# Kernel tuning notes

Hardware: AMD Instinct MI355X
Metric: run time of the kernel (lower is better)

## Reference

```python
import jax, jax.numpy as jnp
import numpy as np

DG = 8   # deformable groups
KK = 9   # 3x3 kernel positions


def conv3x3(x, w, b):
    # x: [B,C,H,W], w: [O,I,3,3] -> SAME conv, stride 1
    y = jax.lax.conv_general_dilated(x, w, (1, 1), 'SAME',
                                     dimension_numbers=('NCHW', 'OIHW', 'NCHW'))
    return y + b[None, :, None, None]


def modulated_deform_conv(x, offset, mask, w, b):
    # x: [B,C,H,W]; offset: [B,DG,KK,2,H,W] (dy,dx per group/kernel-pos);
    # mask: [B,DG,KK,H,W]; w: [O,C,3,3]; groups=1, stride=1, pad=1, dil=1.
    B, C, H, W = x.shape
    cg = C // DG  # channels per deformable group
    dy = offset[:, :, :, 0]  # [B,DG,KK,H,W]
    dx = offset[:, :, :, 1]
    ky, kx = jnp.meshgrid(jnp.arange(3), jnp.arange(3), indexing='ij')
    ky = (ky.reshape(KK) - 1).astype(x.dtype)  # kernel y offsets (pad=1)
    kx = (kx.reshape(KK) - 1).astype(x.dtype)
    py = dy + jnp.arange(H, dtype=x.dtype).reshape(1, 1, 1, H, 1) + ky.reshape(1, 1, KK, 1, 1)
    px = dx + jnp.arange(W, dtype=x.dtype).reshape(1, 1, 1, 1, W) + kx.reshape(1, 1, KK, 1, 1)
    y0 = jnp.floor(py)
    x0 = jnp.floor(px)
    ly = py - y0  # bilinear fractions
    lx = px - x0
    y0i = y0.astype(jnp.int32)
    x0i = x0.astype(jnp.int32)
    xf = x.reshape(B, DG, cg, H * W)

    def gather(yi, xi):
        # zero padding outside the image (per-corner validity)
        valid = ((yi >= 0) & (yi < H) & (xi >= 0) & (xi < W)).astype(x.dtype)
        idx = jnp.clip(yi, 0, H - 1) * W + jnp.clip(xi, 0, W - 1)  # [B,DG,KK,H,W]
        g = jnp.take_along_axis(xf, idx.reshape(B, DG, 1, KK * H * W), axis=-1)
        return g.reshape(B, DG, cg, KK, H, W) * valid[:, :, None]

    v = (((1 - ly) * (1 - lx))[:, :, None] * gather(y0i, x0i)
         + ((1 - ly) * lx)[:, :, None] * gather(y0i, x0i + 1)
         + (ly * (1 - lx))[:, :, None] * gather(y0i + 1, x0i)
         + (ly * lx)[:, :, None] * gather(y0i + 1, x0i + 1))
    v = (v * mask[:, :, None]).reshape(B, C, KK, H, W)  # modulated im2col
    out = jnp.einsum('bckhw,ock->bohw', v, w.reshape(w.shape[0], C, KK))
    return out + b[None, :, None, None]


def setup_inputs() -> dict:
    key = jax.random.key(0)
    ks = jax.random.split(key, 6)
    B, C, H, W = 8, 64, 128, 128
    f = lambda k, s: jax.random.normal(k, s, dtype=jnp.float32)
    return {
        'cat_fea': f(ks[0], (B, C, H, W)),
        'f_fea': f(ks[1], (B, C, H, W)),
        'w_off2d': f(ks[2], (C, C, 3, 3)) * 0.05,
        'b_off2d': jnp.zeros((C,), jnp.float32),
        'w_coff': f(ks[3], (3 * DG * KK, C, 3, 3)) * 0.01,  # small => near-zero offsets, as in DCNv2Pack init
        'b_coff': jnp.zeros((3 * DG * KK,), jnp.float32),
        'w_dconv': f(ks[4], (C, C, 3, 3)) * 0.05,
        'b_dconv': jnp.zeros((C,), jnp.float32),
    }


def reference(cat_fea, f_fea, w_off2d, b_off2d, w_coff, b_coff, w_dconv, b_dconv):
    # offset1 = self.off2d_1(cat_fea)
    offset_feat = conv3x3(cat_fea, w_off2d, b_off2d)
    # DCNv2Pack: conv_offset on the extra feature, chunk into o1,o2,mask
    off = conv3x3(offset_feat, w_coff, b_coff)  # [B, 3*DG*KK, H, W]
    o1, o2, m = jnp.split(off, 3, axis=1)
    B, _, H, W = off.shape
    # offset = cat(o1,o2); CUDA kernel reads channel ((g*KK+i)*2 + {0:y,1:x})
    offset = jnp.concatenate([o1, o2], axis=1).reshape(B, DG, KK, 2, H, W)
    mask = jax.nn.sigmoid(m).reshape(B, DG, KK, H, W)
    return modulated_deform_conv(f_fea, offset, mask, w_dconv, b_dconv)
```

## Files before the change

kernel.cpp:

```cpp
#include <hip/hip_runtime.h>
#include <math.h>

typedef __attribute__((ext_vector_type(4))) float f32x4;
typedef __attribute__((ext_vector_type(8))) short bf16x8;
typedef __attribute__((ext_vector_type(2))) _Float16 f16x2;
typedef __attribute__((ext_vector_type(8))) _Float16 f16x8;

#define HH 128
#define WW 128
#define HWSZ 16384
#define BHW 131072
#define BB 8

__device__ __forceinline__ float bf2f(ushort u) {
    union { uint i; float f; } x; x.i = ((uint)u) << 16; return x.f;
}
__device__ __forceinline__ ushort f2bf(float f) {
    union { float f; uint i; } x; x.f = f;
    uint r = (x.i + 0x7fffu + ((x.i >> 16) & 1u)) >> 16;
    return (ushort)r;
}
__device__ __forceinline__ ushort f2h_bits(float f) {
    union { _Float16 h; ushort u; } x; x.h = (_Float16)f; return x.u;
}

template<int F16>
__global__ __launch_bounds__(256) void to_gp_k(const float* __restrict__ x,
                                               ushort* __restrict__ y) {
    __shared__ ushort lds[64][66];
    int blk = blockIdx.x;
    int b = blk >> 8;
    int hw0 = (blk & 255) << 6;
    int t = threadIdx.x;
    int lane = t & 63;
    int q = t >> 6;
#pragma unroll
    for (int i = 0; i < 16; i++) {
        int c = i * 4 + q;
        float v = x[((size_t)(b * 64 + c) << 14) + hw0 + lane];
        lds[c][lane] = F16 ? f2h_bits(v) : f2bf(v);
    }
    __syncthreads();
#pragma unroll
    for (int it = 0; it < 2; it++) {
        int id = it * 256 + t;
        int cg = id >> 6;
        int px = id & 63;
        uint pk[4];
#pragma unroll
        for (int j = 0; j < 4; j++)
            pk[j] = (uint)lds[cg * 8 + 2 * j][px] | ((uint)lds[cg * 8 + 2 * j + 1][px] << 16);
        *(uint4*)(y + ((((size_t)b * 8 + cg) << 14) + hw0 + px) * 8) = *(uint4*)pk;
    }
}

template<int F16>
__global__ __launch_bounds__(256) void prep_wa(const float* __restrict__ w,
                                               ushort* __restrict__ wa, int Co, int Co_pad) {
    int idx = blockIdx.x * 256 + threadIdx.x;
    if (idx >= Co_pad * 576) return;
    int co = idx / 576, r = idx % 576;
    int kk = r >> 6, ci = r & 63;
    ushort v = 0;
    if (co < Co) {
        float f = w[(co * 64 + ci) * 9 + kk];
        v = F16 ? f2h_bits(f) : f2bf(f);
    }
    wa[idx] = v;
}

template<int NCO, int MODE>
__global__ __launch_bounds__(256, 3) void conv_gemm2_k(
    const ushort* __restrict__ xt, const ushort* __restrict__ wa,
    const float* __restrict__ bias, ushort* __restrict__ y,
    uint* __restrict__ dyxp, ushort* __restrict__ mpl, int Cout) {
    __shared__ ushort Al[NCO * 64 * 64];
    __shared__ ushort Bt[64 * 64];
    int t = threadIdx.x;
    int orig = blockIdx.x;
    int blk = (orig & 7) * 256 + (orig >> 3);
    int b = blk >> 8;
    int h = (blk >> 1) & 127;
    int w0 = (blk & 1) << 6;
    int lane = t & 63;
    int wv = t >> 6;
    int lg = lane >> 4;
    int lr = lane & 15;
    int rs = (lr & 7) << 4;
    int asw = ((lane & 7) ^ (lane >> 3)) << 4;
    const char* wab = (const char*)wa;

    f32x4 acc[NCO][4];
#pragma unroll
    for (int n = 0; n < NCO; n++)
#pragma unroll
        for (int j = 0; j < 4; j++) acc[n][j] = f32x4{0, 0, 0, 0};

#pragma unroll 1
    for (int kk = 0; kk < 9; kk++) {
        int ky = kk / 3;
        int kx = kk - ky * 3;
        __syncthreads();
#pragma unroll
        for (int a = 0; a < 2 * NCO; a++) {
            int rb = wv * (NCO * 16) + a * 8;
            const char* g = wab + (size_t)(rb + (lane >> 3)) * 1152 + kk * 128 + asw;
            __builtin_amdgcn_global_load_lds(
                (const __attribute__((address_space(1))) void*)g,
                (__attribute__((address_space(3))) void*)((char*)Al + rb * 128),
                16, 0, 0);
        }
        int hy = h + ky - 1;
        int wx = w0 + lane + kx - 1;
        bool val = ((unsigned)hy < 128u) && ((unsigned)wx < 128u);
        uint4 v0 = {0u, 0u, 0u, 0u}, v1 = {0u, 0u, 0u, 0u};
        if (val) {
            const ushort* gb = xt + ((((size_t)b * 8 + wv) << 14) + (hy << 7) + wx) * 8;
            v0 = *(const uint4*)gb;
            v1 = *(const uint4*)(gb + (4ull << 17));
        }
        int swl = (lane & 7) << 4;
        *(uint4*)((char*)Bt + lane * 128 + ((wv * 16) ^ swl)) = v0;
        *(uint4*)((char*)Bt + lane * 128 + (((wv + 4) * 16) ^ swl)) = v1;
        __syncthreads();
#pragma unroll
        for (int n = 0; n < NCO; n++) {
            int ar = n * 64 + wv * 16 + lr;
            bf16x8 a0 = *(const bf16x8*)((char*)Al + ar * 128 + ((lg * 16) ^ rs));
            bf16x8 a1 = *(const bf16x8*)((char*)Al + ar * 128 + ((lg * 16 + 64) ^ rs));
#pragma unroll
            for (int j = 0; j < 4; j++) {
                int pr = j * 16 + lr;
                bf16x8 b0 = *(const bf16x8*)((char*)Bt + pr * 128 + ((lg * 16) ^ rs));
                bf16x8 b1 = *(const bf16x8*)((char*)Bt + pr * 128 + ((lg * 16 + 64) ^ rs));
                acc[n][j] = __builtin_amdgcn_mfma_f32_16x16x32_bf16(a0, b0, acc[n][j], 0, 0, 0);
                acc[n][j] = __builtin_amdgcn_mfma_f32_16x16x32_bf16(a1, b1, acc[n][j], 0, 0, 0);
            }
        }
    }

#pragma unroll
    for (int n = 0; n < NCO; n++) {
        int co_g = n * 64 + wv * 16 + lg * 4;
        if (co_g < Cout) {
            float bs[4];
#pragma unroll
            for (int r = 0; r < 4; r++) bs[r] = bias[co_g + r];
#pragma unroll
            for (int j = 0; j < 4; j++) {
                int pxl = j * 16 + lr;
                int hw = (h << 7) + w0 + pxl;
                int bhw = (b << 14) + hw;
                if (MODE == 0) {
                    int cg = co_g >> 3, cs = co_g & 7;
                    uint2 s2;
                    s2.x = (uint)f2bf(acc[n][j][0] + bs[0]) | ((uint)f2bf(acc[n][j][1] + bs[1]) << 16);
                    s2.y = (uint)f2bf(acc[n][j][2] + bs[2]) | ((uint)f2bf(acc[n][j][3] + bs[3]) << 16);
                    *(uint2*)(y + ((((size_t)b * 8 + cg) << 14) + hw) * 8 + cs) = s2;
                } else if (co_g < 144) {
                    int p0 = co_g >> 1;
                    uint u0 = (uint)f2bf(acc[n][j][0] + bs[0]) | ((uint)f2bf(acc[n][j][1] + bs[1]) << 16);
                    uint u1 = (uint)f2bf(acc[n][j][2] + bs[2]) | ((uint)f2bf(acc[n][j][3] + bs[3]) << 16);
                    dyxp[(size_t)p0 * BHW + bhw] = u0;
                    dyxp[(size_t)(p0 + 1) * BHW + bhw] = u1;
                } else {
#pragma unroll
                    for (int r = 0; r < 4; r++) {
                        float f = 1.f / (1.f + __expf(-(acc[n][j][r] + bs[r])));
                        mpl[(size_t)(co_g - 144 + r) * BHW + bhw] = f2bf(f);
                    }
                }
            }
        }
    }
}

__global__ __launch_bounds__(256) void sample_k(
    const ushort* __restrict__ xg, const uint* __restrict__ dyxp,
    const ushort* __restrict__ mpl, ushort* __restrict__ vt) {
    int p = blockIdx.y;
    int dg = p / 9, tap = p - dg * 9;
    int ky = tap / 3, kx = tap - ky * 3;
    int bx = blockIdx.x;
    int bxs = (bx & 7) * 64 + (bx >> 3);
    int bhw = (bxs << 8) + threadIdx.x;
    int b = bhw >> 14;
    int h = (bhw >> 7) & 127;
    int w = bhw & 127;

    uint dyx = dyxp[(size_t)p * BHW + bhw];
    float m = bf2f(mpl[(size_t)p * BHW + bhw]);
    float dy = bf2f((ushort)(dyx & 0xffff));
    float dx = bf2f((ushort)(dyx >> 16));
    float py = dy + (float)(h + ky - 1);
    float px_ = dx + (float)(w + kx - 1);
    float fy = floorf(py), fx = floorf(px_);
    int y0 = (int)fy, x0 = (int)fx;
    int y1 = y0 + 1, x1 = x0 + 1;
    float ly = py - fy, lx = px_ - fx;
    bool vy0 = (unsigned)y0 < 128u, vy1 = (unsigned)y1 < 128u;
    bool vx0 = (unsigned)x0 < 128u, vx1 = (unsigned)x1 < 128u;
    float w00 = (vy0 && vx0) ? (1.f - ly) * (1.f - lx) * m : 0.f;
    float w01 = (vy0 && vx1) ? (1.f - ly) * lx * m : 0.f;
    float w10 = (vy1 && vx0) ? ly * (1.f - lx) * m : 0.f;
    float w11 = (vy1 && vx1) ? ly * lx * m : 0.f;
    int y0c = min(max(y0, 0), 127), y1c = min(max(y1, 0), 127);
    int x0c = min(max(x0, 0), 127), x1c = min(max(x1, 0), 127);
    const ushort* gb = xg + (((size_t)b * 8 + dg) << 17);
    uint4 q00 = *(const uint4*)(gb + ((y0c << 7) + x0c) * 8);
    uint4 q01 = *(const uint4*)(gb + ((y0c << 7) + x1c) * 8);
    uint4 q10 = *(const uint4*)(gb + ((y1c << 7) + x0c) * 8);
    uint4 q11 = *(const uint4*)(gb + ((y1c << 7) + x1c) * 8);
    const ushort* u00 = (const ushort*)&q00;
    const ushort* u01 = (const ushort*)&q01;
    const ushort* u10 = (const ushort*)&q10;
    const ushort* u11 = (const ushort*)&q11;
    uint pk[4];
#pragma unroll
    for (int c2 = 0; c2 < 4; c2++) {
        float v0 = w00 * bf2f(u00[2*c2])   + w01 * bf2f(u01[2*c2])
                 + w10 * bf2f(u10[2*c2])   + w11 * bf2f(u11[2*c2]);
        float v1 = w00 * bf2f(u00[2*c2+1]) + w01 * bf2f(u01[2*c2+1])
                 + w10 * bf2f(u10[2*c2+1]) + w11 * bf2f(u11[2*c2+1]);
        pk[c2] = (uint)f2bf(v0) | ((uint)f2bf(v1) << 16);
    }
    *(uint4*)(vt + ((size_t)p * BHW + bhw) * 8) = *(uint4*)pk;
}

__global__ __launch_bounds__(256, 3) void dgemm_k(
    const ushort* __restrict__ vt, const ushort* __restrict__ wa,
    const float* __restrict__ bias, float* __restrict__ out) {
    __shared__ ushort Al[64 * 64];
    __shared__ ushort Bt[64 * 64];
    int t = threadIdx.x;
    int orig = blockIdx.x;
    int blk = (orig & 7) * 256 + (orig >> 3);
    int b = blk >> 8;
    int h = (blk >> 1) & 127;
    int w0 = (blk & 1) << 6;
    int lane = t & 63;
    int wv = t >> 6;
    int lg = lane >> 4;
    int lr = lane & 15;
    int rs = (lr & 7) << 4;
    int asw = ((lane & 7) ^ (lane >> 3)) << 4;
    const char* wab = (const char*)wa;
    int bhw0 = (b << 14) + (h << 7) + w0;

    f32x4 acc[4] = {f32x4{0,0,0,0}, f32x4{0,0,0,0}, f32x4{0,0,0,0}, f32x4{0,0,0,0}};

#pragma unroll 1
    for (int kk = 0; kk < 9; kk++) {
        __syncthreads();
#pragma unroll
        for (int a = 0; a < 2; a++) {
            int rb = wv * 16 + a * 8;
            const char* g = wab + (size_t)(rb + (lane >> 3)) * 1152 + kk * 128 + asw;
            __builtin_amdgcn_global_load_lds(
                (const __attribute__((address_space(1))) void*)g,
                (__attribute__((address_space(3))) void*)((char*)Al + rb * 128),
                16, 0, 0);
        }
        uint4 v0 = *(const uint4*)(vt + ((size_t)(wv * 9 + kk) * BHW + bhw0 + lane) * 8);
        uint4 v1 = *(const uint4*)(vt + ((size_t)((wv + 4) * 9 + kk) * BHW + bhw0 + lane) * 8);
        int swl = (lane & 7) << 4;
        *(uint4*)((char*)Bt + lane * 128 + ((wv * 16) ^ swl)) = v0;
        *(uint4*)((char*)Bt + lane * 128 + (((wv + 4) * 16) ^ swl)) = v1;
        __syncthreads();
        int ar = wv * 16 + lr;
        bf16x8 a0 = *(const bf16x8*)((char*)Al + ar * 128 + ((lg * 16) ^ rs));
        bf16x8 a1 = *(const bf16x8*)((char*)Al + ar * 128 + ((lg * 16 + 64) ^ rs));
#pragma unroll
        for (int j = 0; j < 4; j++) {
            int pr = j * 16 + lr;
            bf16x8 b0 = *(const bf16x8*)((char*)Bt + pr * 128 + ((lg * 16) ^ rs));
            bf16x8 b1 = *(const bf16x8*)((char*)Bt + pr * 128 + ((lg * 16 + 64) ^ rs));
            acc[j] = __builtin_amdgcn_mfma_f32_16x16x32_bf16(a0, b0, acc[j], 0, 0, 0);
            acc[j] = __builtin_amdgcn_mfma_f32_16x16x32_bf16(a1, b1, acc[j], 0, 0, 0);
        }
    }

    int co_g = wv * 16 + lg * 4;
    float bs[4];
#pragma unroll
    for (int r = 0; r < 4; r++) bs[r] = bias[co_g + r];
#pragma unroll
    for (int j = 0; j < 4; j++) {
        int hw = (h << 7) + w0 + j * 16 + lr;
#pragma unroll
        for (int r = 0; r < 4; r++) {
            out[((size_t)(b * 64 + co_g + r) << 14) + hw] = acc[j][r] + bs[r];
        }
    }
}

__global__ __launch_bounds__(256, 3) void deform_reg3_k(
    const ushort* __restrict__ xg, const uint* __restrict__ dyxp,
    const ushort* __restrict__ mpl, const ushort* __restrict__ wa,
    const float* __restrict__ bias, float* __restrict__ out) {
    int t = threadIdx.x;
    int orig = blockIdx.x;
    int blk = (orig & 7) * 256 + (orig >> 3);
    int b = blk >> 8;
    int h = (blk >> 1) & 127;
    int w0 = (blk & 1) << 6;
    int lane = t & 63;
    int wv = t >> 6;
    int lg = lane >> 4;
    int lr = lane & 15;
    int wabs = w0 + wv * 16 + lr;
    int bhw = (b << 14) + (h << 7) + wabs;

    uint dyxv[18];
    float mv[18];
#pragma unroll
    for (int c = 0; c < 18; c++) {
        int dg = ((c & 1) << 2) + lg;
        int tap = c >> 1;
        dyxv[c] = dyxp[(size_t)(dg * 9 + tap) * BHW + bhw];
        mv[c] = bf2f(mpl[(size_t)(dg * 9 + tap) * BHW + bhw]);
    }

    uint4 qg[2][4];
    f32x4 wt4[2];
    f16x8 afr[2][4];
    f32x4 acc[4] = {f32x4{0,0,0,0}, f32x4{0,0,0,0}, f32x4{0,0,0,0}, f32x4{0,0,0,0}};

#define DPRE(c) do {                                                            \
    const int tap = (c) >> 1;                                                   \
    const int ky = tap / 3;                                                     \
    const int kx = tap - ky * 3;                                                \
    int dg = (((c) & 1) << 2) + lg;                                             \
    uint dyx = dyxv[(c)];                                                       \
    float dy = bf2f((ushort)(dyx & 0xffff));                                    \
    float dx = bf2f((ushort)(dyx >> 16));                                       \
    float py = dy + (float)(h + ky - 1);                                        \
    float px_ = dx + (float)(wabs + kx - 1);                                    \
    float fy = floorf(py), fx = floorf(px_);                                    \
    int y0 = (int)fy, x0 = (int)fx;                                             \
    int y1 = y0 + 1, x1 = x0 + 1;                                               \
    int y0c = min(max(y0, 0), 127), y1c = min(max(y1, 0), 127);                 \
    int x0c = min(max(x0, 0), 127), x1c = min(max(x1, 0), 127);                 \
    const ushort* gb = xg + (((size_t)b * 8 + dg) << 17);                       \
    qg[(c) & 1][0] = *(const uint4*)(gb + ((y0c << 7) + x0c) * 8);              \
    qg[(c) & 1][1] = *(const uint4*)(gb + ((y0c << 7) + x1c) * 8);              \
    qg[(c) & 1][2] = *(const uint4*)(gb + ((y1c << 7) + x0c) * 8);              \
    qg[(c) & 1][3] = *(const uint4*)(gb + ((y1c << 7) + x1c) * 8);              \
    float ly = py - fy, lx = px_ - fx;                                          \
    bool vy0 = (unsigned)y0 < 128u, vy1 = (unsigned)y1 < 128u;                  \
    bool vx0 = (unsigned)x0 < 128u, vx1 = (unsigned)x1 < 128u;                  \
    float m = mv[(c)];                                                          \
    f32x4 wv4;                                                                  \
    wv4[0] = (vy0 && vx0) ? (1.f - ly) * (1.f - lx) * m : 0.f;                  \
    wv4[1] = (vy0 && vx1) ? (1.f - ly) * lx * m : 0.f;                          \
    wv4[2] = (vy1 && vx0) ? ly * (1.f - lx) * m : 0.f;                          \
    wv4[3] = (vy1 && vx1) ? ly * lx * m : 0.f;                                  \
    wt4[(c) & 1] = wv4;                                                         \
} while (0)

#define APRE(c) do {                                                            \
    const ushort* wac = wa + (c) * 32 + lg * 8;                                 \
    _Pragma("unroll")                                                           \
    for (int n = 0; n < 4; n++)                                                 \
        afr[(c) & 1][n] = *(const f16x8*)(wac + (size_t)(n * 16 + lr) * 576);   \
} while (0)

    DPRE(0);
    APRE(0);

#pragma unroll
    for (int c = 0; c < 18; c++) {
        if (c < 17) {
            DPRE(c + 1);
            APRE(c + 1);
        }
        __builtin_amdgcn_sched_barrier(0);
        f32x4 wc = wt4[c & 1];
        _Float16 wh0 = (_Float16)wc[0], wh1 = (_Float16)wc[1];
        _Float16 wh2 = (_Float16)wc[2], wh3 = (_Float16)wc[3];
        f16x2 w0p = {wh0, wh0}, w1p = {wh1, wh1}, w2p = {wh2, wh2}, w3p = {wh3, wh3};
        union { uint4 u4; uint u[4]; } c00, c01, c10, c11;
        c00.u4 = qg[c & 1][0]; c01.u4 = qg[c & 1][1];
        c10.u4 = qg[c & 1][2]; c11.u4 = qg[c & 1][3];
        union { f16x2 p[4]; f16x8 v; } bf;
#pragma unroll
        for (int c2 = 0; c2 < 4; c2++) {
            union { uint u; f16x2 h; } h00, h01, h10, h11;
            h00.u = c00.u[c2]; h01.u = c01.u[c2];
            h10.u = c10.u[c2]; h11.u = c11.u[c2];
            bf.p[c2] = h00.h * w0p + h01.h * w1p + h10.h * w2p + h11.h * w3p;
        }
#pragma unroll
        for (int n = 0; n < 4; n++)
            acc[n] = __builtin_amdgcn_mfma_f32_16x16x32_f16(afr[c & 1][n], bf.v, acc[n], 0, 0, 0);
    }
#undef DPRE
#undef APRE

    int hw = (h << 7) + wabs;
#pragma unroll
    for (int n = 0; n < 4; n++) {
        int co_g = n * 16 + lg * 4;
#pragma unroll
        for (int r = 0; r < 4; r++) {
            out[((size_t)(b * 64 + co_g + r) << 14) + hw] = acc[n][r] + bias[co_g + r];
        }
    }
}

extern "C" void kernel_launch(void* const* d_in, const int* in_sizes, int n_in,
                              void* d_out, int out_size, void* d_ws, size_t ws_size,
                              hipStream_t stream) {
    const float* cat_fea = (const float*)d_in[0];
    const float* f_fea   = (const float*)d_in[1];
    const float* w_off2d = (const float*)d_in[2];
    const float* b_off2d = (const float*)d_in[3];
    const float* w_coff  = (const float*)d_in[4];
    const float* b_coff  = (const float*)d_in[5];
    const float* w_dconv = (const float*)d_in[6];
    const float* b_dconv = (const float*)d_in[7];
    float* out = (float*)d_out;

    const size_t NEED_SG = 224837632ull;

    if (ws_size >= NEED_SG) {
        ushort* xft  = (ushort*)d_ws;
        uint*   dyxp = (uint*)(xft + 8388608);
        ushort* mpl  = (ushort*)(dyxp + 9437184);
        ushort* wa1  = mpl + 9437184;
        ushort* wa2  = wa1 + 36864;
        ushort* wad  = wa2 + 147456;
        ushort* vt   = wad + 36864;
        ushort* x1t      = vt;
        ushort* off_feat = vt + 8388608;

        to_gp_k<0><<<2048, 256, 0, stream>>>(cat_fea, x1t);
        to_gp_k<0><<<2048, 256, 0, stream>>>(f_fea, xft);
        prep_wa<0><<<(64 * 576 + 255) / 256, 256, 0, stream>>>(w_off2d, wa1, 64, 64);
        prep_wa<0><<<(256 * 576 + 255) / 256, 256, 0, stream>>>(w_coff, wa2, 216, 256);
        prep_wa<0><<<(64 * 576 + 255) / 256, 256, 0, stream>>>(w_dconv, wad, 64, 64);

        conv_gemm2_k<1, 0><<<2048, 256, 0, stream>>>(x1t, wa1, b_off2d, off_feat,
                                                     nullptr, nullptr, 64);
        conv_gemm2_k<4, 1><<<2048, 256, 0, stream>>>(off_feat, wa2, b_coff, nullptr,
                                                     dyxp, mpl, 216);
        sample_k<<<dim3(512, 72), 256, 0, stream>>>(xft, dyxp, mpl, vt);
        dgemm_k<<<2048, 256, 0, stream>>>(vt, wad, b_dconv, out);
    } else {
        ushort* x1t      = (ushort*)d_ws;
        ushort* xft      = x1t + 8388608;
        ushort* off_feat = xft + 8388608;
        uint*   dyxp     = (uint*)(off_feat + 8388608);
        ushort* mpl      = (ushort*)(dyxp + 9437184);
        ushort* wa1      = mpl + 9437184;
        ushort* wa2      = wa1 + 36864;
        ushort* wad      = wa2 + 147456;

        to_gp_k<0><<<2048, 256, 0, stream>>>(cat_fea, x1t);
        to_gp_k<1><<<2048, 256, 0, stream>>>(f_fea, xft);
        prep_wa<0><<<(64 * 576 + 255) / 256, 256, 0, stream>>>(w_off2d, wa1, 64, 64);
        prep_wa<0><<<(256 * 576 + 255) / 256, 256, 0, stream>>>(w_coff, wa2, 216, 256);
        prep_wa<1><<<(64 * 576 + 255) / 256, 256, 0, stream>>>(w_dconv, wad, 64, 64);

        conv_gemm2_k<1, 0><<<2048, 256, 0, stream>>>(x1t, wa1, b_off2d, off_feat,
                                                     nullptr, nullptr, 64);
        conv_gemm2_k<4, 1><<<2048, 256, 0, stream>>>(off_feat, wa2, b_coff, nullptr,
                                                     dyxp, mpl, 216);
        deform_reg3_k<<<2048, 256, 0, stream>>>(xft, dyxp, mpl, wad, b_dconv, out);
    }
}
```

Measured before the change: 170.3 us.

## Double-buffer LDS tiles in conv GEMM to overlap loads with MFMA

Splits the LDS A (weights) and B (input patch) tiles in the 3x3 conv GEMM kernel into two buffers. Loads for the next kernel position are issued before the MFMA work on the current one, leaving one barrier per iteration. This aims to hide global-load latency behind compute. In exchange LDS use doubles and launch bounds drop from 3 to 2 blocks per SM, which lowers occupancy and could offset the gain.

Measured after the change: 185.0 us. +8.6%, slower.

```diff
diff --git a/kernel.cpp b/kernel.cpp
--- a/kernel.cpp
+++ b/kernel.cpp
@@ -70,12 +70,13 @@
 }
 
 template<int NCO, int MODE>
-__global__ __launch_bounds__(256, 3) void conv_gemm2_k(
+__global__ __launch_bounds__(256, 2) void conv_gemm2_k(
     const ushort* __restrict__ xt, const ushort* __restrict__ wa,
     const float* __restrict__ bias, ushort* __restrict__ y,
     uint* __restrict__ dyxp, ushort* __restrict__ mpl, int Cout) {
-    __shared__ ushort Al[NCO * 64 * 64];
-    __shared__ ushort Bt[64 * 64];
+    __shared__ ushort Al[2 * NCO * 64 * 64];
+    __shared__ ushort Bt[2 * 64 * 64];
+    const int ASZ = NCO * 8192;
     int t = threadIdx.x;
     int orig = blockIdx.x;
     int blk = (orig & 7) * 256 + (orig >> 3);
@@ -89,55 +90,75 @@
     int rs = (lr & 7) << 4;
     int asw = ((lane & 7) ^ (lane >> 3)) << 4;
     const char* wab = (const char*)wa;
+    uint4 bv0, bv1;
+
+#define STAGE_A(KK, BI) do {                                                    \
+    _Pragma("unroll")                                                           \
+    for (int a = 0; a < 2 * NCO; a++) {                                         \
+        int rb = wv * (NCO * 16) + a * 8;                                       \
+        const char* g = wab + (size_t)(rb + (lane >> 3)) * 1152 + (KK) * 128 + asw; \
+        __builtin_amdgcn_global_load_lds(                                       \
+            (const __attribute__((address_space(1))) void*)g,                   \
+            (__attribute__((address_space(3))) void*)((char*)Al + (BI) * ASZ + rb * 128), \
+            16, 0, 0);                                                          \
+    } } while (0)
+
+#define LOAD_B(KK) do {                                                         \
+    int ky_ = (KK) / 3, kx_ = (KK) - ky_ * 3;                                   \
+    int hy = h + ky_ - 1;                                                       \
+    int wx = w0 + lane + kx_ - 1;                                               \
+    bool val = ((unsigned)hy < 128u) && ((unsigned)wx < 128u);                  \
+    bv0 = uint4{0u, 0u, 0u, 0u}; bv1 = uint4{0u, 0u, 0u, 0u};                   \
+    if (val) {                                                                  \
+        const ushort* gb = xt + ((((size_t)b * 8 + wv) << 14) + (hy << 7) + wx) * 8; \
+        bv0 = *(const uint4*)gb;                                                \
+        bv1 = *(const uint4*)(gb + (4ull << 17));                               \
+    } } while (0)
+
+#define WRITE_B(BI) do {                                                        \
+    int swl = (lane & 7) << 4;                                                  \
+    *(uint4*)((char*)Bt + (BI) * 8192 + lane * 128 + ((wv * 16) ^ swl)) = bv0;  \
+    *(uint4*)((char*)Bt + (BI) * 8192 + lane * 128 + (((wv + 4) * 16) ^ swl)) = bv1; \
+} while (0)
 
     f32x4 acc[NCO][4];
 #pragma unroll
     for (int n = 0; n < NCO; n++)
 #pragma unroll
         for (int j = 0; j < 4; j++) acc[n][j] = f32x4{0, 0, 0, 0};
+
+    LOAD_B(0);
+    STAGE_A(0, 0);
+    WRITE_B(0);
+    __syncthreads();
 
 #pragma unroll 1
     for (int kk = 0; kk < 9; kk++) {
-        int ky = kk / 3;
-        int kx = kk - ky * 3;
-        __syncthreads();
-#pragma unroll
-        for (int a = 0; a < 2 * NCO; a++) {
-            int rb = wv * (NCO * 16) + a * 8;
-            const char* g = wab + (size_t)(rb + (lane >> 3)) * 1152 + kk * 128 + asw;
-            __builtin_amdgcn_global_load_lds(
-                (const __attribute__((address_space(1))) void*)g,
-                (__attribute__((address_space(3))) void*)((char*)Al + rb * 128),
-                16, 0, 0);
-        }
-        int hy = h + ky - 1;
-        int wx = w0 + lane + kx - 1;
-        bool val = ((unsigned)hy < 128u) && ((unsigned)wx < 128u);
-        uint4 v0 = {0u, 0u, 0u, 0u}, v1 = {0u, 0u, 0u, 0u};
-        if (val) {
-            const ushort* gb = xt + ((((size_t)b * 8 + wv) << 14) + (hy << 7) + wx) * 8;
-            v0 = *(const uint4*)gb;
-            v1 = *(const uint4*)(gb + (4ull << 17));
-        }
-        int swl = (lane & 7) << 4;
-        *(uint4*)((char*)Bt + lane * 128 + ((wv * 16) ^ swl)) = v0;
-        *(uint4*)((char*)Bt + lane * 128 + (((wv + 4) * 16) ^ swl)) = v1;
-        __syncthreads();
+        int bi = kk & 1;
+        if (kk < 8) {
+            LOAD_B(kk + 1);
+            STAGE_A(kk + 1, bi ^ 1);
+        }
 #pragma unroll
         for (int n = 0; n < NCO; n++) {
             int ar = n * 64 + wv * 16 + lr;
-            bf16x8 a0 = *(const bf16x8*)((char*)Al + ar * 128 + ((lg * 16) ^ rs));
-            bf16x8 a1 = *(const bf16x8*)((char*)Al + ar * 128 + ((lg * 16 + 64) ^ rs));
+            bf16x8 a0 = *(const bf16x8*)((char*)Al + bi * ASZ + ar * 128 + ((lg * 16) ^ rs));
+            bf16x8 a1 = *(const bf16x8*)((char*)Al + bi * ASZ + ar * 128 + ((lg * 16 + 64) ^ rs));
 #pragma unroll
             for (int j = 0; j < 4; j++) {
                 int pr = j * 16 + lr;
-                bf16x8 b0 = *(const bf16x8*)((char*)Bt + pr * 128 + ((lg * 16) ^ rs));
-                bf16x8 b1 = *(const bf16x8*)((char*)Bt + pr * 128 + ((lg * 16 + 64) ^ rs));
+                bf16x8 b0 = *(const bf16x8*)((char*)Bt + bi * 8192 + pr * 128 + ((lg * 16) ^ rs));
+                bf16x8 b1 = *(const bf16x8*)((char*)Bt + bi * 8192 + pr * 128 + ((lg * 16 + 64) ^ rs));
                 acc[n][j] = __builtin_amdgcn_mfma_f32_16x16x32_bf16(a0, b0, acc[n][j], 0, 0, 0);
                 acc[n][j] = __builtin_amdgcn_mfma_f32_16x16x32_bf16(a1, b1, acc[n][j], 0, 0, 0);
             }
         }
-    }
+        if (kk < 8) WRITE_B(bi ^ 1);
+        __syncthreads();
+    }
+#undef STAGE_A
+#undef LOAD_B
+#undef WRITE_B
 
 #pragma unroll
     for (int n = 0; n < NCO; n++) {
```

## Retile conv GEMM to full-row pixel tiles and split output channels across grid

Applied to the files above, without the earlier changes.

The im2col conv GEMM now processes a full 128-pixel image row per block instead of 64 pixels, and the 256-channel offset conv is split over two blockIdx.y output-channel tiles of 128 each. Each wave holds its A fragments in registers and reuses every B fragment across its channel sub-tiles, raising MFMA work per LDS read. Occupancy target rises to 4 blocks per CU. The pixel tile is twice as large and the LDS layout changes, which trades more LDS and register pressure for fewer blocks and more reuse.

Measured after the change: 170.6 us. About the same (+0.2%).

```diff
diff --git a/kernel.cpp b/kernel.cpp
--- a/kernel.cpp
+++ b/kernel.cpp
@@ -69,19 +69,22 @@
     wa[idx] = v;
 }
 
-template<int NCO, int MODE>
-__global__ __launch_bounds__(256, 3) void conv_gemm2_k(
+template<int COT, int MODE>
+__global__ __launch_bounds__(256, 4) void conv_gemm3_k(
     const ushort* __restrict__ xt, const ushort* __restrict__ wa,
     const float* __restrict__ bias, ushort* __restrict__ y,
     uint* __restrict__ dyxp, ushort* __restrict__ mpl, int Cout) {
-    __shared__ ushort Al[NCO * 64 * 64];
-    __shared__ ushort Bt[64 * 64];
+    constexpr int WCO = COT / 4;
+    constexpr int NN = WCO / 16;
+    constexpr int NA = COT / 32;
+    __shared__ ushort Al[COT * 64];
+    __shared__ ushort Bt[128 * 64];
     int t = threadIdx.x;
     int orig = blockIdx.x;
-    int blk = (orig & 7) * 256 + (orig >> 3);
-    int b = blk >> 8;
-    int h = (blk >> 1) & 127;
-    int w0 = (blk & 1) << 6;
+    int blk = (orig & 7) * 128 + (orig >> 3);
+    int b = blk >> 7;
+    int h = blk & 127;
+    int cot = blockIdx.y;
     int lane = t & 63;
     int wv = t >> 6;
     int lg = lane >> 4;
@@ -90,11 +93,11 @@
     int asw = ((lane & 7) ^ (lane >> 3)) << 4;
     const char* wab = (const char*)wa;
 
-    f32x4 acc[NCO][4];
-#pragma unroll
-    for (int n = 0; n < NCO; n++)
-#pragma unroll
-        for (int j = 0; j < 4; j++) acc[n][j] = f32x4{0, 0, 0, 0};
+    f32x4 acc[NN][8];
+#pragma unroll
+    for (int n = 0; n < NN; n++)
+#pragma unroll
+        for (int j = 0; j < 8; j++) acc[n][j] = f32x4{0, 0, 0, 0};
 
 #pragma unroll 1
     for (int kk = 0; kk < 9; kk++) {
@@ -102,54 +105,59 @@
         int kx = kk - ky * 3;
         __syncthreads();
 #pragma unroll
-        for (int a = 0; a < 2 * NCO; a++) {
-            int rb = wv * (NCO * 16) + a * 8;
-            const char* g = wab + (size_t)(rb + (lane >> 3)) * 1152 + kk * 128 + asw;
+        for (int a = 0; a < NA; a++) {
+            int rb = wv * WCO + a * 8;
+            const char* g = wab + (size_t)(cot * COT + rb + (lane >> 3)) * 1152 + kk * 128 + asw;
             __builtin_amdgcn_global_load_lds(
                 (const __attribute__((address_space(1))) void*)g,
                 (__attribute__((address_space(3))) void*)((char*)Al + rb * 128),
                 16, 0, 0);
         }
         int hy = h + ky - 1;
-        int wx = w0 + lane + kx - 1;
-        bool val = ((unsigned)hy < 128u) && ((unsigned)wx < 128u);
-        uint4 v0 = {0u, 0u, 0u, 0u}, v1 = {0u, 0u, 0u, 0u};
-        if (val) {
-            const ushort* gb = xt + ((((size_t)b * 8 + wv) << 14) + (hy << 7) + wx) * 8;
-            v0 = *(const uint4*)gb;
-            v1 = *(const uint4*)(gb + (4ull << 17));
-        }
-        int swl = (lane & 7) << 4;
-        *(uint4*)((char*)Bt + lane * 128 + ((wv * 16) ^ swl)) = v0;
-        *(uint4*)((char*)Bt + lane * 128 + (((wv + 4) * 16) ^ swl)) = v1;
+        bool vr = (unsigned)hy < 128u;
+#pragma unroll
+        for (int i = 0; i < 4; i++) {
+            int id = i * 256 + t;
+            int px = id & 127;
+            int cg = id >> 7;
+            int wx = px + kx - 1;
+            uint4 v = {0u, 0u, 0u, 0u};
+            if (vr && (unsigned)wx < 128u)
+                v = *(const uint4*)(xt + ((((size_t)b * 8 + cg) << 14) + (hy << 7) + wx) * 8);
+            *(uint4*)((char*)Bt + px * 128 + ((cg * 16) ^ ((px & 7) << 4))) = v;
+        }
         __syncthreads();
-#pragma unroll
-        for (int n = 0; n < NCO; n++) {
-            int ar = n * 64 + wv * 16 + lr;
-            bf16x8 a0 = *(const bf16x8*)((char*)Al + ar * 128 + ((lg * 16) ^ rs));
-            bf16x8 a1 = *(const bf16x8*)((char*)Al + ar * 128 + ((lg * 16 + 64) ^ rs));
-#pragma unroll
-            for (int j = 0; j < 4; j++) {
-                int pr = j * 16 + lr;
-                bf16x8 b0 = *(const bf16x8*)((char*)Bt + pr * 128 + ((lg * 16) ^ rs));
-                bf16x8 b1 = *(const bf16x8*)((char*)Bt + pr * 128 + ((lg * 16 + 64) ^ rs));
-                acc[n][j] = __builtin_amdgcn_mfma_f32_16x16x32_bf16(a0, b0, acc[n][j], 0, 0, 0);
-                acc[n][j] = __builtin_amdgcn_mfma_f32_16x16x32_bf16(a1, b1, acc[n][j], 0, 0, 0);
+        bf16x8 a0[NN], a1[NN];
+#pragma unroll
+        for (int n = 0; n < NN; n++) {
+            int ar = wv * WCO + n * 16 + lr;
+            a0[n] = *(const bf16x8*)((char*)Al + ar * 128 + ((lg * 16) ^ rs));
+            a1[n] = *(const bf16x8*)((char*)Al + ar * 128 + ((lg * 16 + 64) ^ rs));
+        }
+#pragma unroll
+        for (int j = 0; j < 8; j++) {
+            int pr = j * 16 + lr;
+            bf16x8 b0 = *(const bf16x8*)((char*)Bt + pr * 128 + ((lg * 16) ^ rs));
+            bf16x8 b1 = *(const bf16x8*)((char*)Bt + pr * 128 + ((lg * 16 + 64) ^ rs));
+#pragma unroll
+            for (int n = 0; n < NN; n++) {
+                acc[n][j] = __builtin_amdgcn_mfma_f32_16x16x32_bf16(a0[n], b0, acc[n][j], 0, 0, 0);
+                acc[n][j] = __builtin_amdgcn_mfma_f32_16x16x32_bf16(a1[n], b1, acc[n][j], 0, 0, 0);
             }
         }
     }
 
 #pragma unroll
-    for (int n = 0; n < NCO; n++) {
-        int co_g = n * 64 + wv * 16 + lg * 4;
+    for (int n = 0; n < NN; n++) {
+        int co_g = cot * COT + wv * WCO + n * 16 + lg * 4;
         if (co_g < Cout) {
             float bs[4];
 #pragma unroll
             for (int r = 0; r < 4; r++) bs[r] = bias[co_g + r];
 #pragma unroll
-            for (int j = 0; j < 4; j++) {
+            for (int j = 0; j < 8; j++) {
                 int pxl = j * 16 + lr;
-                int hw = (h << 7) + w0 + pxl;
+                int hw = (h << 7) + pxl;
                 int bhw = (b << 14) + hw;
                 if (MODE == 0) {
                     int cg = co_g >> 3, cs = co_g & 7;
@@ -440,10 +448,10 @@
         prep_wa<0><<<(256 * 576 + 255) / 256, 256, 0, stream>>>(w_coff, wa2, 216, 256);
         prep_wa<0><<<(64 * 576 + 255) / 256, 256, 0, stream>>>(w_dconv, wad, 64, 64);
 
-        conv_gemm2_k<1, 0><<<2048, 256, 0, stream>>>(x1t, wa1, b_off2d, off_feat,
-                                                     nullptr, nullptr, 64);
-        conv_gemm2_k<4, 1><<<2048, 256, 0, stream>>>(off_feat, wa2, b_coff, nullptr,
-                                                     dyxp, mpl, 216);
+        conv_gemm3_k<64, 0><<<dim3(1024, 1), 256, 0, stream>>>(x1t, wa1, b_off2d, off_feat,
+                                                               nullptr, nullptr, 64);
+        conv_gemm3_k<128, 1><<<dim3(1024, 2), 256, 0, stream>>>(off_feat, wa2, b_coff, nullptr,
+                                                                dyxp, mpl, 216);
         sample_k<<<dim3(512, 72), 256, 0, stream>>>(xft, dyxp, mpl, vt);
         dgemm_k<<<2048, 256, 0, stream>>>(vt, wad, b_dconv, out);
     } else {
@@ -462,10 +470,10 @@
         prep_wa<0><<<(256 * 576 + 255) / 256, 256, 0, stream>>>(w_coff, wa2, 216, 256);
         prep_wa<1><<<(64 * 576 + 255) / 256, 256, 0, stream>>>(w_dconv, wad, 64, 64);
 
-        conv_gemm2_k<1, 0><<<2048, 256, 0, stream>>>(x1t, wa1, b_off2d, off_feat,
-                                                     nullptr, nullptr, 64);
-        conv_gemm2_k<4, 1><<<2048, 256, 0, stream>>>(off_feat, wa2, b_coff, nullptr,
-                                                     dyxp, mpl, 216);
+        conv_gemm3_k<64, 0><<<dim3(1024, 1), 256, 0, stream>>>(x1t, wa1, b_off2d, off_feat,
+                                                               nullptr, nullptr, 64);
+        conv_gemm3_k<128, 1><<<dim3(1024, 2), 256, 0, stream>>>(off_feat, wa2, b_coff, nullptr,
+                                                                dyxp, mpl, 216);
         deform_reg3_k<<<2048, 256, 0, stream>>>(xft, dyxp, mpl, wad, b_dconv, out);
     }
 }
```
